# Kernel optimization log

Measured on AMD Instinct MI355X. Metric: run time of the kernel, lower is better.

Reference implementation:

```python
import jax, jax.numpy as jnp
import numpy as np

DIM = 128
HEADS = 4
K = 7          # neighborhood kernel size
MLP_RATIO = 4
EPS = 1e-5


def setup_inputs() -> dict:
    key = jax.random.key(0)
    ks = jax.random.split(key, 8)
    B, H, W, C = 4, 64, 64, DIM
    hid = C * MLP_RATIO
    s = lambda k, shape: jax.random.normal(k, shape, jnp.float32) * 0.02
    return {
        "x": jax.random.normal(ks[0], (B, H, W, C), jnp.float32),
        "ln1_g": jnp.ones((C,), jnp.float32),
        "ln1_b": jnp.zeros((C,), jnp.float32),
        "qkv_w": s(ks[1], (C, 3 * C)),
        "qkv_b": jnp.zeros((3 * C,), jnp.float32),
        "rpb": s(ks[2], (HEADS, 2 * K - 1, 2 * K - 1)),
        "proj_w": s(ks[3], (C, C)),
        "proj_b": jnp.zeros((C,), jnp.float32),
        "ln2_g": jnp.ones((C,), jnp.float32),
        "ln2_b": jnp.zeros((C,), jnp.float32),
        "fc1_w": s(ks[4], (C, hid)),
        "fc1_b": jnp.zeros((hid,), jnp.float32),
        "fc2_w": s(ks[5], (hid, C)),
        "fc2_b": jnp.zeros((C,), jnp.float32),
    }


def _ln(x, g, b):
    m = jnp.mean(x, axis=-1, keepdims=True)
    v = jnp.mean(jnp.square(x - m), axis=-1, keepdims=True)
    return (x - m) * jax.lax.rsqrt(v + EPS) * g + b


def _neigh_idx(L, k):
    # NATTEN border-clamped neighborhood: start = clamp(i - k//2, 0, L-k)
    i = jnp.arange(L)
    start = jnp.clip(i - k // 2, 0, L - k)
    idx = start[:, None] + jnp.arange(k)[None, :]        # [L, k] key positions
    rel = idx - i[:, None] + (k - 1)                     # [L, k] rpb indices in [0, 2k-2]
    return idx, rel


def _neighborhood_attention(x, qkv_w, qkv_b, rpb, proj_w, proj_b):
    B, H, W, C = x.shape
    nh, hd = HEADS, C // HEADS
    scale = hd ** -0.5
    qkv = (x @ qkv_w + qkv_b).reshape(B, H, W, 3, nh, hd)
    qkv = qkv.transpose(3, 0, 4, 1, 2, 5)                # [3, B, nh, H, W, hd]
    q, k_, v = qkv[0] * scale, qkv[1], qkv[2]
    ih, rh = _neigh_idx(H, K)
    iw, rw = _neigh_idx(W, K)
    # gather 7x7 neighborhoods: [B, nh, H, K, W, K, hd]
    kg = k_[:, :, ih][:, :, :, :, iw]
    vg = v[:, :, ih][:, :, :, :, iw]
    attn = jnp.einsum('bnywc,bnykxjc->bnyxkj', q, kg)    # [B, nh, H, W, K, K]
    bias = rpb[:, rh][:, :, :, rw]                       # [nh, H, K, W, K]
    attn = attn + bias.transpose(0, 1, 3, 2, 4)[None]
    a = jax.nn.softmax(attn.reshape(B, nh, H, W, K * K), axis=-1)
    a = a.reshape(B, nh, H, W, K, K)
    out = jnp.einsum('bnyxkj,bnykxjc->bnyxc', a, vg)     # [B, nh, H, W, hd]
    out = out.transpose(0, 2, 3, 1, 4).reshape(B, H, W, C)
    return out @ proj_w + proj_b


def reference(x, ln1_g, ln1_b, qkv_w, qkv_b, rpb, proj_w, proj_b,
              ln2_g, ln2_b, fc1_w, fc1_b, fc2_w, fc2_b):
    h = x + _neighborhood_attention(_ln(x, ln1_g, ln1_b), qkv_w, qkv_b, rpb, proj_w, proj_b)
    y = _ln(h, ln2_g, ln2_b)
    y = jax.nn.gelu(y @ fc1_w + fc1_b, approximate=False) @ fc2_w + fc2_b
    return h + y
```

## Files before the change

### kernel.cpp

```cpp
#include <hip/hip_runtime.h>
#include <math.h>

#define TOKS 16384
#define CDIM 128
#define NH 4
#define HD 32
#define HID 512
#define QSCALE 0.17677669529663687f
#define LEPS 1e-5f

typedef const float* fp;
typedef const unsigned short* bfp16;
typedef __attribute__((ext_vector_type(8))) short bf16x8;
typedef __attribute__((ext_vector_type(4))) float f32x4;

__device__ inline unsigned int bfp2(float a, float b) {
    unsigned int ua = __float_as_uint(a); ua = (ua + 0x7FFFu + ((ua >> 16) & 1u)) >> 16;
    unsigned int ub = __float_as_uint(b); ub = (ub + 0x7FFFu + ((ub >> 16) & 1u)) >> 16;
    return ua | (ub << 16);
}
__device__ inline unsigned short bf1(float a) {
    unsigned int u = __float_as_uint(a);
    return (unsigned short)((u + 0x7FFFu + ((u >> 16) & 1u)) >> 16);
}
__device__ inline float lo16(unsigned int u) { return __uint_as_float(u << 16); }
__device__ inline float hi16(unsigned int u) { return __uint_as_float(u & 0xFFFF0000u); }

__global__ __launch_bounds__(256) void prep(fp qw, fp pw, fp f1w, fp f2w,
                                            unsigned short* __restrict__ wt) {
    int e = blockIdx.x * 256 + threadIdx.x;
    float v;
    if (e < 49152) { int n = e >> 7, k = e & 127; v = qw[(size_t)k * 384 + n]; }
    else if (e < 65536) {
        int i = e - 49152;
        int frag = i >> 9, w = i & 511, lane = w >> 3, el = w & 7;
        int rt = frag >> 2, kk = frag & 3;
        int row = rt * 16 + (lane & 15);
        int k = kk * 32 + (lane >> 4) * 8 + el;
        v = pw[(size_t)k * 128 + row];
    } else if (e < 131072) {
        int i = e - 65536;
        int frag = i >> 9, w = i & 511, lane = w >> 3, el = w & 7;
        int rt = frag >> 2, kk = frag & 3;
        int row = rt * 16 + (lane & 15);
        int k = kk * 32 + (lane >> 4) * 8 + el;
        v = f1w[(size_t)k * 512 + row];
    } else {
        int i = e - 131072;
        int frag = i >> 9, w = i & 511, lane = w >> 3, el = w & 7;
        int rt = frag >> 4, kc = frag & 15;
        int row = rt * 16 + (lane & 15);
        int k = kc * 32 + (lane >> 4) * 8 + el;
        v = f2w[(size_t)k * 128 + row];
    }
    wt[e] = bf1(v);
}

__global__ __launch_bounds__(256) void k1_mfma(fp x, fp g1, fp b1, bfp16 wt0, fp wb,
                                               float* __restrict__ qb,
                                               unsigned short* __restrict__ kvb) {
    __shared__ unsigned int lds[12288];
    const int m0 = blockIdx.x * 128;
    const int nb = blockIdx.y * 64;
    const int tid = threadIdx.x;
#pragma unroll
    for (int i = 0; i < 8; i++) {
        int slot = tid + i * 256;
        int m = slot >> 4, c16 = slot & 15;
        const float4 v0 = *(const float4*)(x + (size_t)(m0 + m) * CDIM + c16 * 8);
        const float4 v1 = *(const float4*)(x + (size_t)(m0 + m) * CDIM + c16 * 8 + 4);
        float s = v0.x + v0.y + v0.z + v0.w + v1.x + v1.y + v1.z + v1.w;
        float q = v0.x * v0.x + v0.y * v0.y + v0.z * v0.z + v0.w * v0.w
                + v1.x * v1.x + v1.y * v1.y + v1.z * v1.z + v1.w * v1.w;
#pragma unroll
        for (int mm = 8; mm >= 1; mm >>= 1) { s += __shfl_xor(s, mm); q += __shfl_xor(q, mm); }
        float mu = s * (1.f / 128.f);
        float rs = rsqrtf(q * (1.f / 128.f) - mu * mu + LEPS);
        const float4 ga = *(const float4*)(g1 + c16 * 8);
        const float4 gb = *(const float4*)(g1 + c16 * 8 + 4);
        const float4 ba = *(const float4*)(b1 + c16 * 8);
        const float4 bb = *(const float4*)(b1 + c16 * 8 + 4);
        uint4 o;
        o.x = bfp2((v0.x - mu) * rs * ga.x + ba.x, (v0.y - mu) * rs * ga.y + ba.y);
        o.y = bfp2((v0.z - mu) * rs * ga.z + ba.z, (v0.w - mu) * rs * ga.w + ba.w);
        o.z = bfp2((v1.x - mu) * rs * gb.x + bb.x, (v1.y - mu) * rs * gb.y + bb.y);
        o.w = bfp2((v1.z - mu) * rs * gb.z + bb.z, (v1.w - mu) * rs * gb.w + bb.w);
        *(uint4*)&lds[m * 64 + ((c16 ^ (m & 15)) << 2)] = o;
    }
#pragma unroll
    for (int i = 0; i < 4; i++) {
        int slot = tid + i * 256;
        int n = slot >> 4, c16 = slot & 15;
        const uint4 v4 = *(const uint4*)(wt0 + (size_t)(nb + n) * 128 + c16 * 8);
        *(uint4*)&lds[8192 + n * 64 + (c16 ^ (n & 15)) * 4] = v4;
    }
    __syncthreads();

    const int lane = tid & 63, wid = tid >> 6, quad = lane >> 4, l16 = lane & 15;
    f32x4 acc[2][4];
#pragma unroll
    for (int mt = 0; mt < 2; mt++)
#pragma unroll
        for (int nt = 0; nt < 4; nt++) acc[mt][nt] = (f32x4){0.f, 0.f, 0.f, 0.f};
#pragma unroll
    for (int kk = 0; kk < 4; kk++) {
        int c = kk * 4 + quad;
        bf16x8 a0 = *(bf16x8*)&lds[(wid * 32 + l16) * 64 + (c ^ l16) * 4];
        bf16x8 a1 = *(bf16x8*)&lds[(wid * 32 + 16 + l16) * 64 + (c ^ l16) * 4];
#pragma unroll
        for (int nt = 0; nt < 4; nt++) {
            bf16x8 bf = *(bf16x8*)&lds[8192 + (nt * 16 + l16) * 64 + (c ^ l16) * 4];
            acc[0][nt] = __builtin_amdgcn_mfma_f32_16x16x32_bf16(a0, bf, acc[0][nt], 0, 0, 0);
            acc[1][nt] = __builtin_amdgcn_mfma_f32_16x16x32_bf16(a1, bf, acc[1][nt], 0, 0, 0);
        }
    }
#pragma unroll
    for (int nt = 0; nt < 4; nt++) {
        int col = nb + nt * 16 + l16;
        float bias = wb[col];
#pragma unroll
        for (int mt = 0; mt < 2; mt++)
#pragma unroll
            for (int r = 0; r < 4; r++) {
                int row = m0 + wid * 32 + mt * 16 + quad * 4 + r;
                float vres = acc[mt][nt][r] + bias;
                if (col < 128)
                    qb[(size_t)row * 128 + col] = vres * QSCALE;
                else if (col < 256)
                    kvb[(size_t)row * 256 + (col - 128)] = bf1(vres);
                else
                    kvb[(size_t)row * 256 + 128 + (col - 256)] = bf1(vres);
            }
    }
}

__global__ __launch_bounds__(256) void k2_attn(const float* __restrict__ qb,
                                               const unsigned short* __restrict__ kvb,
                                               fp rpb, unsigned short* __restrict__ attnb) {
    __shared__ unsigned int lds[12544];
    const int blk = blockIdx.x;
    const int hp = blk & 1;
    const int tile = blk >> 1;
    const int bb = tile >> 6;
    const int ty0 = ((tile >> 3) & 7) << 3;
    const int tx0 = (tile & 7) << 3;
    const int ry0 = min(max(ty0 - 3, 0), 50);
    const int rx0 = min(max(tx0 - 3, 0), 50);
    const int tid = threadIdx.x;

#pragma unroll
    for (int it = 0; it < 13; it++) {
        int slot = it * 256 + tid;
        if (slot < 3136) {
            int r = slot >> 4, c = slot & 15;
            int i = r / 14, j = r - i * 14;
            size_t tok = (size_t)((bb << 12) + (ry0 + i) * 64 + rx0 + j);
            int off = (c < 8) ? (hp * 64 + c * 8) : (128 + hp * 64 + (c - 8) * 8);
            const uint4 v = *(const uint4*)(kvb + tok * 256 + off);
            *(uint4*)&lds[r * 64 + ((c ^ (r & 7)) << 2)] = v;
        }
    }

    const int dh = tid & 1;
    const int hl = (tid >> 1) & 1;
    const int t = tid >> 2;
    const int head = hp * 2 + hl;
    const int tx = t & 7, ty = t >> 3;
    const int y = ty0 + ty, x = tx0 + tx;
    const int token = (bb << 12) + y * 64 + x;
    const int sy = min(max(y - 3, 0), 57);
    const int sx = min(max(x - 3, 0), 57);
    const int ib = sy - ry0, jb = sx - rx0;
    const float* rp = rpb + head * 169 + (sy - y + 6) * 13 + (sx - x + 6);
    const int cbK = hl * 4 + dh * 2;
    const int cbV = 8 + cbK;

    float q[16];
    {
        const float4* qp = (const float4*)(qb + (size_t)token * 128 + head * 32 + dh * 16);
        float4 a = qp[0], b = qp[1], c = qp[2], d = qp[3];
        q[0] = a.x; q[1] = a.y; q[2] = a.z; q[3] = a.w;
        q[4] = b.x; q[5] = b.y; q[6] = b.z; q[7] = b.w;
        q[8] = c.x; q[9] = c.y; q[10] = c.z; q[11] = c.w;
        q[12] = d.x; q[13] = d.y; q[14] = d.z; q[15] = d.w;
    }
    __syncthreads();

    float s[49];
    float mx = -1e30f;
#pragma unroll
    for (int dy = 0; dy < 7; dy++) {
#pragma unroll
        for (int dx = 0; dx < 7; dx++) {
            int r = (ib + dy) * 14 + jb + dx;
            int sw = r & 7;
            const uint4 k0 = *(const uint4*)&lds[r * 64 + ((cbK ^ sw) << 2)];
            const uint4 k1 = *(const uint4*)&lds[r * 64 + (((cbK + 1) ^ sw) << 2)];
            float ss = q[0] * lo16(k0.x) + q[1] * hi16(k0.x)
                     + q[2] * lo16(k0.y) + q[3] * hi16(k0.y)
                     + q[4] * lo16(k0.z) + q[5] * hi16(k0.z)
                     + q[6] * lo16(k0.w) + q[7] * hi16(k0.w)
                     + q[8] * lo16(k1.x) + q[9] * hi16(k1.x)
                     + q[10] * lo16(k1.y) + q[11] * hi16(k1.y)
                     + q[12] * lo16(k1.z) + q[13] * hi16(k1.z)
                     + q[14] * lo16(k1.w) + q[15] * hi16(k1.w);
            ss += __shfl_xor(ss, 1);
            float sc = ss + rp[dy * 13 + dx];
            s[dy * 7 + dx] = sc;
            mx = fmaxf(mx, sc);
        }
    }
    float sum = 0.f;
#pragma unroll
    for (int i = 0; i < 49; i++) { s[i] = __expf(s[i] - mx); sum += s[i]; }
    float inv = 1.f / sum;

    float o[16];
#pragma unroll
    for (int i2 = 0; i2 < 16; i2++) o[i2] = 0.f;
#pragma unroll
    for (int dy = 0; dy < 7; dy++) {
#pragma unroll
        for (int dx = 0; dx < 7; dx++) {
            int r = (ib + dy) * 14 + jb + dx;
            int sw = r & 7;
            const uint4 v0 = *(const uint4*)&lds[r * 64 + ((cbV ^ sw) << 2)];
            const uint4 v1 = *(const uint4*)&lds[r * 64 + (((cbV + 1) ^ sw) << 2)];
            float p = s[dy * 7 + dx];
            o[0] += p * lo16(v0.x); o[1] += p * hi16(v0.x);
            o[2] += p * lo16(v0.y); o[3] += p * hi16(v0.y);
            o[4] += p * lo16(v0.z); o[5] += p * hi16(v0.z);
            o[6] += p * lo16(v0.w); o[7] += p * hi16(v0.w);
            o[8] += p * lo16(v1.x); o[9] += p * hi16(v1.x);
            o[10] += p * lo16(v1.y); o[11] += p * hi16(v1.y);
            o[12] += p * lo16(v1.z); o[13] += p * hi16(v1.z);
            o[14] += p * lo16(v1.w); o[15] += p * hi16(v1.w);
        }
    }
    unsigned short* op = attnb + (size_t)token * 128 + head * 32 + dh * 16;
    uint4 ov;
    ov.x = bfp2(o[0] * inv, o[1] * inv); ov.y = bfp2(o[2] * inv, o[3] * inv);
    ov.z = bfp2(o[4] * inv, o[5] * inv); ov.w = bfp2(o[6] * inv, o[7] * inv);
    *(uint4*)op = ov;
    ov.x = bfp2(o[8] * inv, o[9] * inv); ov.y = bfp2(o[10] * inv, o[11] * inv);
    ov.z = bfp2(o[12] * inv, o[13] * inv); ov.w = bfp2(o[14] * inv, o[15] * inv);
    *(uint4*)(op + 8) = ov;
}

__global__ __launch_bounds__(512) void kpm4(bfp16 attnb, fp x, bfp16 wt1, fp pb,
                                            fp g2, fp b2, bfp16 wt2, fp b1v,
                                            bfp16 wt3, fp b2v, float* __restrict__ out) {
    __shared__ unsigned int lds[12288];
    float* ldsf = (float*)lds;
    unsigned short* ldsu = (unsigned short*)lds;
    const int m0 = blockIdx.x * 32;
    const int tid = threadIdx.x;
    const int lane = tid & 63, wid = tid >> 6, quad = lane >> 4, l16 = lane & 15;

    {
        int m = tid >> 4, c16 = tid & 15;
        const uint4 v4 = *(const uint4*)(attnb + (size_t)(m0 + m) * CDIM + c16 * 8);
        *(uint4*)&lds[m * 64 + ((c16 ^ (m & 15)) << 2)] = v4;
    }
    __syncthreads();

    const int mt = wid & 1, nhf = wid >> 1;
    f32x4 pacc[2];
#pragma unroll
    for (int nt = 0; nt < 2; nt++) pacc[nt] = (f32x4){0.f, 0.f, 0.f, 0.f};
#pragma unroll
    for (int kk = 0; kk < 4; kk++) {
        int c = kk * 4 + quad;
        bf16x8 a = *(bf16x8*)&lds[(mt * 16 + l16) * 64 + ((c ^ l16) << 2)];
#pragma unroll
        for (int nt = 0; nt < 2; nt++) {
            int rt = nhf * 2 + nt;
            bf16x8 bf = *(const bf16x8*)(wt1 + (size_t)((rt * 4 + kk) * 64 + lane) * 8);
            pacc[nt] = __builtin_amdgcn_mfma_f32_16x16x32_bf16(a, bf, pacc[nt], 0, 0, 0);
        }
    }
    float sr[4] = {0.f, 0.f, 0.f, 0.f}, qr[4] = {0.f, 0.f, 0.f, 0.f};
#pragma unroll
    for (int nt = 0; nt < 2; nt++) {
        int col = nhf * 32 + nt * 16 + l16;
        float bias = pb[col];
#pragma unroll
        for (int r = 0; r < 4; r++) {
            int lrow = mt * 16 + quad * 4 + r;
            float hv = x[(size_t)(m0 + lrow) * CDIM + col] + pacc[nt][r] + bias;
            pacc[nt][r] = hv;
            sr[r] += hv; qr[r] += hv * hv;
        }
    }
#pragma unroll
    for (int mm = 1; mm <= 8; mm <<= 1) {
#pragma unroll
        for (int r = 0; r < 4; r++) {
            sr[r] += __shfl_xor(sr[r], mm);
            qr[r] += __shfl_xor(qr[r], mm);
        }
    }
    __syncthreads();
    if (l16 == 0) {
#pragma unroll
        for (int r = 0; r < 4; r++) {
            ldsf[wid * 32 + (quad * 4 + r) * 2]     = sr[r];
            ldsf[wid * 32 + (quad * 4 + r) * 2 + 1] = qr[r];
        }
    }
    __syncthreads();
    float mu[4], rs[4];
#pragma unroll
    for (int r = 0; r < 4; r++) {
        float st = 0.f, qt = 0.f;
#pragma unroll
        for (int p = 0; p < 4; p++) {
            int w2 = p * 2 + mt;
            st += ldsf[w2 * 32 + (quad * 4 + r) * 2];
            qt += ldsf[w2 * 32 + (quad * 4 + r) * 2 + 1];
        }
        mu[r] = st * (1.f / 128.f);
        rs[r] = rsqrtf(qt * (1.f / 128.f) - mu[r] * mu[r] + LEPS);
    }
#pragma unroll
    for (int nt = 0; nt < 2; nt++) {
        int col = nhf * 32 + nt * 16 + l16;
        float gg = g2[col], bbv = b2[col];
        int c16h = col >> 3, cw = col & 7;
#pragma unroll
        for (int r = 0; r < 4; r++) {
            int lrow = mt * 16 + quad * 4 + r;
            ldsu[4096 + lrow * 128 + ((c16h ^ (lrow & 15)) << 3) + cw] =
                bf1((pacc[nt][r] - mu[r]) * rs[r] * gg + bbv);
        }
    }
    __syncthreads();

#pragma unroll
    for (int ht = 0; ht < 4; ht++) {
        f32x4 acc0 = (f32x4){0.f, 0.f, 0.f, 0.f};
        f32x4 acc1 = (f32x4){0.f, 0.f, 0.f, 0.f};
#pragma unroll
        for (int kk = 0; kk < 4; kk++) {
            int c = kk * 4 + quad;
            bf16x8 wf = *(const bf16x8*)(wt2 + (size_t)(((wid * 4 + ht) * 4 + kk) * 64 + lane) * 8);
            bf16x8 x0 = *(bf16x8*)&lds[2048 + l16 * 64 + ((c ^ l16) << 2)];
            bf16x8 x1 = *(bf16x8*)&lds[2048 + (16 + l16) * 64 + ((c ^ l16) << 2)];
            acc0 = __builtin_amdgcn_mfma_f32_16x16x32_bf16(wf, x0, acc0, 0, 0, 0);
            acc1 = __builtin_amdgcn_mfma_f32_16x16x32_bf16(wf, x1, acc1, 0, 0, 0);
        }
        const int hidb = wid * 64 + ht * 16 + quad * 4;
        const float4 bb = *(const float4*)(b1v + hidb);
        const int c16y = hidb >> 3;
        const int woff = (quad & 1) << 1;
#pragma unroll
        for (int t = 0; t < 2; t++) {
            f32x4 a = t ? acc1 : acc0;
            int row = t * 16 + l16;
            float z0 = a[0] + bb.x, z1 = a[1] + bb.y, z2 = a[2] + bb.z, z3 = a[3] + bb.w;
            float g0 = 0.5f * z0 * (1.f + erff(z0 * 0.70710678118654752f));
            float g1 = 0.5f * z1 * (1.f + erff(z1 * 0.70710678118654752f));
            float g2v = 0.5f * z2 * (1.f + erff(z2 * 0.70710678118654752f));
            float g3 = 0.5f * z3 * (1.f + erff(z3 * 0.70710678118654752f));
            uint2 val; val.x = bfp2(g0, g1); val.y = bfp2(g2v, g3);
            *(uint2*)&lds[4096 + row * 256 + ((c16y ^ (row & 15)) << 2) + woff] = val;
        }
    }
    __syncthreads();

    f32x4 facc[2];
#pragma unroll
    for (int nt = 0; nt < 2; nt++) facc[nt] = (f32x4){0.f, 0.f, 0.f, 0.f};
#pragma unroll
    for (int kc = 0; kc < 16; kc++) {
        int c = kc * 4 + quad;
        bf16x8 a = *(bf16x8*)&lds[4096 + (mt * 16 + l16) * 256 + ((c ^ l16) << 2)];
#pragma unroll
        for (int nt = 0; nt < 2; nt++) {
            int rt = nhf * 2 + nt;
            bf16x8 bf = *(const bf16x8*)(wt3 + (size_t)((rt * 16 + kc) * 64 + lane) * 8);
            facc[nt] = __builtin_amdgcn_mfma_f32_16x16x32_bf16(a, bf, facc[nt], 0, 0, 0);
        }
    }
#pragma unroll
    for (int nt = 0; nt < 2; nt++) {
        int col = nhf * 32 + nt * 16 + l16;
        float bias = b2v[col];
#pragma unroll
        for (int r = 0; r < 4; r++) {
            int lrow = mt * 16 + quad * 4 + r;
            out[(size_t)(m0 + lrow) * CDIM + col] = pacc[nt][r] + facc[nt][r] + bias;
        }
    }
}

extern "C" void kernel_launch(void* const* d_in, const int* in_sizes, int n_in,
                              void* d_out, int out_size, void* d_ws, size_t ws_size,
                              hipStream_t stream) {
    fp x      = (fp)d_in[0];
    fp ln1_g  = (fp)d_in[1];
    fp ln1_b  = (fp)d_in[2];
    fp qkv_w  = (fp)d_in[3];
    fp qkv_b  = (fp)d_in[4];
    fp rpb    = (fp)d_in[5];
    fp proj_w = (fp)d_in[6];
    fp proj_b = (fp)d_in[7];
    fp ln2_g  = (fp)d_in[8];
    fp ln2_b  = (fp)d_in[9];
    fp fc1_w  = (fp)d_in[10];
    fp fc1_b  = (fp)d_in[11];
    fp fc2_w  = (fp)d_in[12];
    fp fc2_b  = (fp)d_in[13];
    float* out = (float*)d_out;

    float* ws = (float*)d_ws;
    float* h  = ws;
    unsigned short* xn = (unsigned short*)(h + (size_t)TOKS * CDIM);
    unsigned short* hn = xn + (size_t)TOKS * CDIM;
    float* qb = (float*)(hn + (size_t)TOKS * CDIM);
    unsigned short* kvb   = (unsigned short*)(qb + (size_t)TOKS * CDIM);
    unsigned short* attnb = kvb + (size_t)TOKS * 256;
    unsigned short* wt    = attnb + (size_t)TOKS * CDIM;

    unsigned short* wt0 = wt;
    unsigned short* wt1 = wt + 49152;
    unsigned short* wt2 = wt + 65536;
    unsigned short* wt3 = wt + 131072;

    prep<<<768, 256, 0, stream>>>(qkv_w, proj_w, fc1_w, fc2_w, wt);
    k1_mfma<<<dim3(TOKS / 128, 6), 256, 0, stream>>>(x, ln1_g, ln1_b, wt0, qkv_b, qb, kvb);
    k2_attn<<<TOKS / 64 * 2, 256, 0, stream>>>(qb, kvb, rpb, attnb);
    kpm4<<<TOKS / 32, 512, 0, stream>>>(attnb, x, wt1, proj_b, ln2_g, ln2_b,
                                        wt2, fc1_b, wt3, fc2_b, out);
}
```

Before: 131.9 us.

## Compute neighborhood attention with MFMA over full 14x14 key halo per tile

Rewrites the attention kernel to use bf16 MFMA for both QK^T and PV. Each block now handles one head for an 8x8 query tile and scores every query against the whole 14x14 halo of 196 keys, padded to 224, masking out keys outside its 7x7 window. V is stored transposed in LDS and the probabilities go through LDS as bf16 for the second MFMA. This swaps scalar FMA dot products for matrix-core work at the cost of about 4.5x redundant score computation, extra masking and LDS traffic, bf16 rounding of q and the probabilities, and a larger LDS footprint.

```diff
diff --git a/kernel.cpp b/kernel.cpp
--- a/kernel.cpp
+++ b/kernel.cpp
@@ -137,114 +137,130 @@
 __global__ __launch_bounds__(256) void k2_attn(const float* __restrict__ qb,
                                                const unsigned short* __restrict__ kvb,
                                                fp rpb, unsigned short* __restrict__ attnb) {
-    __shared__ unsigned int lds[12544];
+    __shared__ unsigned int lds[15616];
+    unsigned short* ldsu = (unsigned short*)lds;
     const int blk = blockIdx.x;
-    const int hp = blk & 1;
-    const int tile = blk >> 1;
+    const int head = blk & 3;
+    const int tile = blk >> 2;
     const int bb = tile >> 6;
     const int ty0 = ((tile >> 3) & 7) << 3;
     const int tx0 = (tile & 7) << 3;
     const int ry0 = min(max(ty0 - 3, 0), 50);
     const int rx0 = min(max(tx0 - 3, 0), 50);
     const int tid = threadIdx.x;
-
-#pragma unroll
-    for (int it = 0; it < 13; it++) {
+    const int base = bb << 12;
+
+#pragma unroll
+    for (int it = 0; it < 4; it++) {
         int slot = it * 256 + tid;
-        if (slot < 3136) {
-            int r = slot >> 4, c = slot & 15;
-            int i = r / 14, j = r - i * 14;
-            size_t tok = (size_t)((bb << 12) + (ry0 + i) * 64 + rx0 + j);
-            int off = (c < 8) ? (hp * 64 + c * 8) : (128 + hp * 64 + (c - 8) * 8);
-            const uint4 v = *(const uint4*)(kvb + tok * 256 + off);
-            *(uint4*)&lds[r * 64 + ((c ^ (r & 7)) << 2)] = v;
-        }
-    }
-
-    const int dh = tid & 1;
-    const int hl = (tid >> 1) & 1;
-    const int t = tid >> 2;
-    const int head = hp * 2 + hl;
-    const int tx = t & 7, ty = t >> 3;
-    const int y = ty0 + ty, x = tx0 + tx;
-    const int token = (bb << 12) + y * 64 + x;
+        if (slot < 784) {
+            int r = slot >> 2, c = slot & 3;
+            int i = (r * 9363) >> 17, j = r - i * 14;
+            size_t tok = (size_t)(base + (ry0 + i) * 64 + rx0 + j);
+            const uint4 kk4 = *(const uint4*)(kvb + tok * 256 + head * 32 + c * 8);
+            *(uint4*)&lds[r * 20 + c * 4] = kk4;
+            const uint4 vv4 = *(const uint4*)(kvb + tok * 256 + 128 + head * 32 + c * 8);
+            unsigned int vv[4] = {vv4.x, vv4.y, vv4.z, vv4.w};
+#pragma unroll
+            for (int e = 0; e < 4; e++) {
+                int d0 = c * 8 + e * 2;
+                ldsu[8960 + d0 * 232 + r] = (unsigned short)(vv[e] & 0xFFFFu);
+                ldsu[8960 + (d0 + 1) * 232 + r] = (unsigned short)(vv[e] >> 16);
+            }
+        }
+    }
+#pragma unroll
+    for (int it = 0; it < 2; it++) {
+        int slot = it * 256 + tid;
+        if (slot < 448) {
+            int d = (slot * 9363) >> 17;
+            int cu = slot - d * 14;
+            lds[4480 + d * 116 + 98 + cu] = 0;
+        }
+    }
+    __syncthreads();
+
+    const int lane = tid & 63, wid = tid >> 6, quad = lane >> 4, l16 = lane & 15;
+    const int q = wid * 16 + l16;
+    const int y = ty0 + (q >> 3), x = tx0 + (q & 7);
+    const int token = base + y * 64 + x;
     const int sy = min(max(y - 3, 0), 57);
     const int sx = min(max(x - 3, 0), 57);
     const int ib = sy - ry0, jb = sx - rx0;
     const float* rp = rpb + head * 169 + (sy - y + 6) * 13 + (sx - x + 6);
-    const int cbK = hl * 4 + dh * 2;
-    const int cbV = 8 + cbK;
-
-    float q[16];
+
+    bf16x8 qf;
     {
-        const float4* qp = (const float4*)(qb + (size_t)token * 128 + head * 32 + dh * 16);
-        float4 a = qp[0], b = qp[1], c = qp[2], d = qp[3];
-        q[0] = a.x; q[1] = a.y; q[2] = a.z; q[3] = a.w;
-        q[4] = b.x; q[5] = b.y; q[6] = b.z; q[7] = b.w;
-        q[8] = c.x; q[9] = c.y; q[10] = c.z; q[11] = c.w;
-        q[12] = d.x; q[13] = d.y; q[14] = d.z; q[15] = d.w;
-    }
-    __syncthreads();
-
-    float s[49];
+        const float* qp = qb + (size_t)token * 128 + head * 32 + quad * 8;
+        union { unsigned int u[4]; bf16x8 v; } pk;
+#pragma unroll
+        for (int e = 0; e < 4; e++) pk.u[e] = bfp2(qp[e * 2], qp[e * 2 + 1]);
+        qf = pk.v;
+    }
+
+    f32x4 accS[14];
+#pragma unroll
+    for (int mt = 0; mt < 14; mt++) {
+        bf16x8 kf = *(bf16x8*)&ldsu[(mt * 16 + l16) * 40 + quad * 8];
+        accS[mt] = __builtin_amdgcn_mfma_f32_16x16x32_bf16(
+            kf, qf, (f32x4){0.f, 0.f, 0.f, 0.f}, 0, 0, 0);
+    }
     float mx = -1e30f;
 #pragma unroll
-    for (int dy = 0; dy < 7; dy++) {
-#pragma unroll
-        for (int dx = 0; dx < 7; dx++) {
-            int r = (ib + dy) * 14 + jb + dx;
-            int sw = r & 7;
-            const uint4 k0 = *(const uint4*)&lds[r * 64 + ((cbK ^ sw) << 2)];
-            const uint4 k1 = *(const uint4*)&lds[r * 64 + (((cbK + 1) ^ sw) << 2)];
-            float ss = q[0] * lo16(k0.x) + q[1] * hi16(k0.x)
-                     + q[2] * lo16(k0.y) + q[3] * hi16(k0.y)
-                     + q[4] * lo16(k0.z) + q[5] * hi16(k0.z)
-                     + q[6] * lo16(k0.w) + q[7] * hi16(k0.w)
-                     + q[8] * lo16(k1.x) + q[9] * hi16(k1.x)
-                     + q[10] * lo16(k1.y) + q[11] * hi16(k1.y)
-                     + q[12] * lo16(k1.z) + q[13] * hi16(k1.z)
-                     + q[14] * lo16(k1.w) + q[15] * hi16(k1.w);
-            ss += __shfl_xor(ss, 1);
-            float sc = ss + rp[dy * 13 + dx];
-            s[dy * 7 + dx] = sc;
-            mx = fmaxf(mx, sc);
-        }
-    }
+    for (int mt = 0; mt < 14; mt++) {
+#pragma unroll
+        for (int rg = 0; rg < 4; rg++) {
+            int r = mt * 16 + quad * 4 + rg;
+            int i = (r * 9363) >> 17;
+            int j = r - i * 14;
+            int di = i - ib, dj = j - jb;
+            bool ok = ((unsigned)di < 7u) && ((unsigned)dj < 7u);
+            float sv = ok ? (accS[mt][rg] + rp[di * 13 + dj]) : -1e30f;
+            accS[mt][rg] = sv;
+            mx = fmaxf(mx, sv);
+        }
+    }
+    mx = fmaxf(mx, __shfl_xor(mx, 16));
+    mx = fmaxf(mx, __shfl_xor(mx, 32));
     float sum = 0.f;
 #pragma unroll
-    for (int i = 0; i < 49; i++) { s[i] = __expf(s[i] - mx); sum += s[i]; }
+    for (int mt = 0; mt < 14; mt++)
+#pragma unroll
+        for (int rg = 0; rg < 4; rg++) {
+            float e = __expf(accS[mt][rg] - mx);
+            accS[mt][rg] = e;
+            sum += e;
+        }
+    sum += __shfl_xor(sum, 16);
+    sum += __shfl_xor(sum, 32);
     float inv = 1.f / sum;
-
-    float o[16];
-#pragma unroll
-    for (int i2 = 0; i2 < 16; i2++) o[i2] = 0.f;
-#pragma unroll
-    for (int dy = 0; dy < 7; dy++) {
-#pragma unroll
-        for (int dx = 0; dx < 7; dx++) {
-            int r = (ib + dy) * 14 + jb + dx;
-            int sw = r & 7;
-            const uint4 v0 = *(const uint4*)&lds[r * 64 + ((cbV ^ sw) << 2)];
-            const uint4 v1 = *(const uint4*)&lds[r * 64 + (((cbV + 1) ^ sw) << 2)];
-            float p = s[dy * 7 + dx];
-            o[0] += p * lo16(v0.x); o[1] += p * hi16(v0.x);
-            o[2] += p * lo16(v0.y); o[3] += p * hi16(v0.y);
-            o[4] += p * lo16(v0.z); o[5] += p * hi16(v0.z);
-            o[6] += p * lo16(v0.w); o[7] += p * hi16(v0.w);
-            o[8] += p * lo16(v1.x); o[9] += p * hi16(v1.x);
-            o[10] += p * lo16(v1.y); o[11] += p * hi16(v1.y);
-            o[12] += p * lo16(v1.z); o[13] += p * hi16(v1.z);
-            o[14] += p * lo16(v1.w); o[15] += p * hi16(v1.w);
-        }
-    }
-    unsigned short* op = attnb + (size_t)token * 128 + head * 32 + dh * 16;
-    uint4 ov;
-    ov.x = bfp2(o[0] * inv, o[1] * inv); ov.y = bfp2(o[2] * inv, o[3] * inv);
-    ov.z = bfp2(o[4] * inv, o[5] * inv); ov.w = bfp2(o[6] * inv, o[7] * inv);
-    *(uint4*)op = ov;
-    ov.x = bfp2(o[8] * inv, o[9] * inv); ov.y = bfp2(o[10] * inv, o[11] * inv);
-    ov.z = bfp2(o[12] * inv, o[13] * inv); ov.w = bfp2(o[14] * inv, o[15] * inv);
-    *(uint4*)(op + 8) = ov;
+#pragma unroll
+    for (int mt = 0; mt < 14; mt++) {
+        uint2 pv;
+        pv.x = bfp2(accS[mt][0] * inv, accS[mt][1] * inv);
+        pv.y = bfp2(accS[mt][2] * inv, accS[mt][3] * inv);
+        *(uint2*)&ldsu[16384 + q * 232 + mt * 16 + quad * 4] = pv;
+    }
+    __syncthreads();
+
+    f32x4 o0 = (f32x4){0.f, 0.f, 0.f, 0.f};
+    f32x4 o1 = (f32x4){0.f, 0.f, 0.f, 0.f};
+#pragma unroll
+    for (int kc = 0; kc < 7; kc++) {
+        bf16x8 pa = *(bf16x8*)&ldsu[16384 + (wid * 16 + l16) * 232 + kc * 32 + quad * 8];
+        bf16x8 v0 = *(bf16x8*)&ldsu[8960 + l16 * 232 + kc * 32 + quad * 8];
+        bf16x8 v1 = *(bf16x8*)&ldsu[8960 + (16 + l16) * 232 + kc * 32 + quad * 8];
+        o0 = __builtin_amdgcn_mfma_f32_16x16x32_bf16(pa, v0, o0, 0, 0, 0);
+        o1 = __builtin_amdgcn_mfma_f32_16x16x32_bf16(pa, v1, o1, 0, 0, 0);
+    }
+#pragma unroll
+    for (int rg = 0; rg < 4; rg++) {
+        int qo = wid * 16 + quad * 4 + rg;
+        int toko = base + (ty0 + (qo >> 3)) * 64 + tx0 + (qo & 7);
+        unsigned short* op = attnb + (size_t)toko * 128 + head * 32;
+        op[l16] = bf1(o0[rg]);
+        op[16 + l16] = bf1(o1[rg]);
+    }
 }
 
 __global__ __launch_bounds__(512) void kpm4(bfp16 attnb, fp x, bfp16 wt1, fp pb,
@@ -429,7 +445,7 @@
 
     prep<<<768, 256, 0, stream>>>(qkv_w, proj_w, fc1_w, fc2_w, wt);
     k1_mfma<<<dim3(TOKS / 128, 6), 256, 0, stream>>>(x, ln1_g, ln1_b, wt0, qkv_b, qb, kvb);
-    k2_attn<<<TOKS / 64 * 2, 256, 0, stream>>>(qb, kvb, rpb, attnb);
+    k2_attn<<<TOKS / 64 * NH, 256, 0, stream>>>(qb, kvb, rpb, attnb);
     kpm4<<<TOKS / 32, 512, 0, stream>>>(attnb, x, wt1, proj_b, ln2_g, ln2_b,
                                         wt2, fc1_b, wt3, fc2_b, out);
 }
```

New measurement: 133.6 us. No clear change (+1.3%).
